# Kernel tuning notes

Hardware: AMD Instinct MI355X
Metric: run time of the kernel (lower is better)

The kernel has to match this reference:

```python
import jax, jax.numpy as jnp
import numpy as np
from jax import lax

STRIDE = 2
PAD = 1
KT = 3   # conv_transpose kernel
KP = 6   # fused pool window/stride (2*3)

def setup_inputs() -> dict:
    key = jax.random.key(0)
    kx, kw, kb = jax.random.split(key, 3)
    x = jax.random.normal(kx, (8, 32, 32, 32, 32), dtype=jnp.float32)
    W = jax.random.normal(kw, (32, 16, KT, KT, KT), dtype=jnp.float32) * 0.05
    b = jax.random.normal(kb, (16,), dtype=jnp.float32) * 0.05
    return {"x": x, "W": W, "b": b}

def _conv_transpose3d(x, W, b):
    # PyTorch conv_transpose3d: weight (C_in, C_out, k, k, k)
    # equivalent to conv with lhs dilation, flipped kernel, swapped I/O axes
    w2 = jnp.flip(W, axis=(2, 3, 4)).swapaxes(0, 1)  # (C_out, C_in, k, k, k)
    pad = KT - 1 - PAD
    y = lax.conv_general_dilated(
        x, w2,
        window_strides=(1, 1, 1),
        padding=[(pad, pad)] * 3,
        lhs_dilation=(STRIDE, STRIDE, STRIDE),
        dimension_numbers=("NCDHW", "OIDHW", "NCDHW"),
    )
    return y + b[None, :, None, None, None]

def reference(x, W, b):
    y = _conv_transpose3d(x, W, b)  # (N, C_out, 63, 63, 63)
    # fused maxpool(k=2,s=2) + maxpool(k=3,s=3) == maxpool(k=6,s=6)
    pooled = lax.reduce_window(
        y, -jnp.inf, lax.max,
        window_dimensions=(1, 1, KP, KP, KP),
        window_strides=(1, 1, KP, KP, KP),
        padding="VALID",
    )  # (N, C_out, 10, 10, 10)
    return jnp.sum(pooled, axis=1, keepdims=True)  # (N, 1, 10, 10, 10)
```

## Files before the change

kernel.cpp:

```cpp
#include <hip/hip_runtime.h>

typedef __bf16 bf16;
typedef __bf16 bf16x8 __attribute__((ext_vector_type(8)));
typedef float f32x4 __attribute__((ext_vector_type(4)));

#define CI_STRIDE 40
#define IW_STRIDE (CI_STRIDE)
#define IH_STRIDE (17 * CI_STRIDE)
#define ID_STRIDE (5 * 17 * CI_STRIDE)
#define XS_ELEMS (4 * ID_STRIDE)

__global__ void transpose_w_kernel(const float* __restrict__ W, bf16* __restrict__ Wt) {
  int o = blockIdx.x * 256 + threadIdx.x;
  if (o < 27 * 512) {
    int j = o & 7, co = (o >> 3) & 15, q = (o >> 7) & 3, tap = o >> 9;
    int ci = q * 8 + j;
    Wt[o] = (bf16)W[(ci * 16 + co) * 27 + tap];
  }
}

__global__ __launch_bounds__(128) void fused_mfma_kernel(
    const float* __restrict__ x, const bf16* __restrict__ Wt,
    const float* __restrict__ b, float* __restrict__ out) {
  __shared__ __align__(16) bf16 xs[XS_ELEMS];
  __shared__ float red[5][2][16];

  const int t = threadIdx.x;
  const int lane = t & 63;
  const int wv = t >> 6;
  const int co = lane & 15;
  const int quad = lane >> 4;

  const int blk = blockIdx.x;
  const int nodoh = blk >> 1;
  const int half = blk & 1;
  const int n = nodoh / 100;
  const int od = (nodoh / 10) % 10;
  const int oh = nodoh % 10;

  bf16x8 bfrag[27];
  {
    const bf16x8* wp = (const bf16x8*)Wt;
#pragma unroll
    for (int tap = 0; tap < 27; ++tap)
      bfrag[tap] = wp[(tap * 4 + quad) * 16 + co];
  }

  {
    const float* xn = x + (size_t)n * (32 * 32768) + (3 * od) * 1024 + (3 * oh) * 32 + 15 * half;
    for (int i = t; i < 512 * 16; i += 128) {
      int w = i & 15;
      int row = i >> 4;
      int ci = row >> 4, ld = (row >> 2) & 3, lh = row & 3;
      float v = xn[ci * 32768 + ld * 1024 + lh * 32 + w];
      xs[(size_t)ld * ID_STRIDE + lh * IH_STRIDE + w * IW_STRIDE + ci] = (bf16)v;
    }
  }
  __syncthreads();

  for (int i = 0; i < 5; ++i) {
    const int tau = wv + 2 * i;
    const int w5 = tau >> 1;
    const int tb = (tau & 1) * 16;

    int pos = tb + (lane & 15);
    if (pos > 26) pos = 26;
    const int md = pos / 9;
    const int rem = pos - md * 9;
    const int mh = rem / 3;
    const int mw = rem - mh * 3;
    const bf16* ap = xs + (size_t)md * ID_STRIDE + mh * IH_STRIDE +
                     (3 * w5 + mw) * IW_STRIDE + quad * 8;

    bf16x8 af[8];
#pragma unroll
    for (int dd = 0; dd < 2; ++dd)
#pragma unroll
      for (int dh = 0; dh < 2; ++dh)
#pragma unroll
        for (int dw = 0; dw < 2; ++dw)
          af[dd * 4 + dh * 2 + dw] =
              *(const bf16x8*)(ap + dd * ID_STRIDE + dh * IH_STRIDE + dw * IW_STRIDE);

    float tmax = -3.4e38f;
#pragma unroll
    for (int pd = 0; pd < 2; ++pd)
#pragma unroll
      for (int ph = 0; ph < 2; ++ph)
#pragma unroll
        for (int pw = 0; pw < 2; ++pw) {
          f32x4 acc = {0.f, 0.f, 0.f, 0.f};
#pragma unroll
          for (int td = 0; td <= pd; ++td)
#pragma unroll
            for (int th = 0; th <= ph; ++th)
#pragma unroll
              for (int tw = 0; tw <= pw; ++tw) {
                const int kd = pd ? (td ? 2 : 0) : 1;
                const int kh = ph ? (th ? 2 : 0) : 1;
                const int kw = pw ? (tw ? 2 : 0) : 1;
                const int tap = kd * 9 + kh * 3 + kw;
                const int ai = ((kd == 0) ? 4 : 0) + ((kh == 0) ? 2 : 0) + ((kw == 0) ? 1 : 0);
                acc = __builtin_amdgcn_mfma_f32_16x16x32_bf16(af[ai], bfrag[tap], acc, 0, 0, 0);
              }
#pragma unroll
          for (int r = 0; r < 4; ++r) {
            if (tb + quad * 4 + r < 27) tmax = fmaxf(tmax, acc[r]);
          }
        }

    tmax = fmaxf(tmax, __shfl_xor(tmax, 16, 64));
    tmax = fmaxf(tmax, __shfl_xor(tmax, 32, 64));
    if (quad == 0) red[w5][tau & 1][co] = tmax;
  }
  __syncthreads();

  if (t < 80) {
    const int w5 = t >> 4;
    const int c = t & 15;
    float v = fmaxf(red[w5][0][c], red[w5][1][c]) + b[c];
    v += __shfl_xor(v, 1, 64);
    v += __shfl_xor(v, 2, 64);
    v += __shfl_xor(v, 4, 64);
    v += __shfl_xor(v, 8, 64);
    if (c == 0) out[nodoh * 10 + half * 5 + w5] = v;
  }
}

extern "C" void kernel_launch(void* const* d_in, const int* in_sizes, int n_in,
                              void* d_out, int out_size, void* d_ws, size_t ws_size,
                              hipStream_t stream) {
  const float* x = (const float*)d_in[0];
  const float* W = (const float*)d_in[1];
  const float* b = (const float*)d_in[2];
  float* out = (float*)d_out;
  bf16* Wt = (bf16*)d_ws;

  transpose_w_kernel<<<dim3(54), dim3(256), 0, stream>>>(W, Wt);
  fused_mfma_kernel<<<dim3(1600), dim3(128), 0, stream>>>(x, Wt, b, out);
}
```

Before: 98.28 us.

## Merge half-width blocks into full-row 256-thread blocks with vectorized LDS staging

Each block now covers the full 32-wide input row (all 10 output columns) with 4 waves instead of two blocks covering halves with 2 waves. This removes the overlapping halo load between the two halves. Each wave keeps a fixed M-tile, so position decoding is hoisted out of the loop. The staging loop now gathers 8 channels per thread and writes one bf16x8 to LDS instead of scalar bf16 stores. The cost is half as many blocks (800) and twice the LDS per block, which may lower occupancy or parallelism.

```diff
diff --git a/kernel.cpp b/kernel.cpp
--- a/kernel.cpp
+++ b/kernel.cpp
@@ -4,26 +4,24 @@
 typedef __bf16 bf16x8 __attribute__((ext_vector_type(8)));
 typedef float f32x4 __attribute__((ext_vector_type(4)));
 
-#define CI_STRIDE 40
-#define IW_STRIDE (CI_STRIDE)
-#define IH_STRIDE (17 * CI_STRIDE)
-#define ID_STRIDE (5 * 17 * CI_STRIDE)
-#define XS_ELEMS (4 * ID_STRIDE)
+#define W_STRIDE 40
+#define H_STRIDE (33 * W_STRIDE)
+#define D_STRIDE (5 * H_STRIDE)
+#define XS_ELEMS (4 * D_STRIDE)
 
 __global__ void transpose_w_kernel(const float* __restrict__ W, bf16* __restrict__ Wt) {
   int o = blockIdx.x * 256 + threadIdx.x;
   if (o < 27 * 512) {
     int j = o & 7, co = (o >> 3) & 15, q = (o >> 7) & 3, tap = o >> 9;
-    int ci = q * 8 + j;
-    Wt[o] = (bf16)W[(ci * 16 + co) * 27 + tap];
+    Wt[o] = (bf16)W[((q * 8 + j) * 16 + co) * 27 + tap];
   }
 }
 
-__global__ __launch_bounds__(128) void fused_mfma_kernel(
+__global__ __launch_bounds__(256) void fused_mfma_kernel(
     const float* __restrict__ x, const bf16* __restrict__ Wt,
     const float* __restrict__ b, float* __restrict__ out) {
   __shared__ __align__(16) bf16 xs[XS_ELEMS];
-  __shared__ float red[5][2][16];
+  __shared__ float red[10][2][16];
 
   const int t = threadIdx.x;
   const int lane = t & 63;
@@ -32,11 +30,9 @@
   const int quad = lane >> 4;
 
   const int blk = blockIdx.x;
-  const int nodoh = blk >> 1;
-  const int half = blk & 1;
-  const int n = nodoh / 100;
-  const int od = (nodoh / 10) % 10;
-  const int oh = nodoh % 10;
+  const int n = blk / 100;
+  const int od = (blk / 10) % 10;
+  const int oh = blk % 10;
 
   bf16x8 bfrag[27];
   {
@@ -47,30 +43,35 @@
   }
 
   {
-    const float* xn = x + (size_t)n * (32 * 32768) + (3 * od) * 1024 + (3 * oh) * 32 + 15 * half;
-    for (int i = t; i < 512 * 16; i += 128) {
-      int w = i & 15;
-      int row = i >> 4;
-      int ci = row >> 4, ld = (row >> 2) & 3, lh = row & 3;
-      float v = xn[ci * 32768 + ld * 1024 + lh * 32 + w];
-      xs[(size_t)ld * ID_STRIDE + lh * IH_STRIDE + w * IW_STRIDE + ci] = (bf16)v;
+    const float* xn = x + (size_t)n * (32 * 32768) + (3 * od) * 1024 + (3 * oh) * 32;
+#pragma unroll 2
+    for (int it = 0; it < 8; ++it) {
+      const int flat = it * 256 + t;
+      const int w = flat & 31;
+      const int row = flat >> 5;
+      const int cig = row & 3;
+      const int lh = (row >> 2) & 3;
+      const int ld = row >> 4;
+      const float* g = xn + (size_t)(cig * 8) * 32768 + ld * 1024 + lh * 32 + w;
+      bf16x8 pk;
+#pragma unroll
+      for (int j = 0; j < 8; ++j) pk[j] = (bf16)g[(size_t)j * 32768];
+      *(bf16x8*)&xs[ld * D_STRIDE + lh * H_STRIDE + w * W_STRIDE + cig * 8] = pk;
     }
   }
   __syncthreads();
 
+  const int tile = wv >> 1;
+  const int tb = tile * 16;
+  int pos = tb + (lane & 15);
+  if (pos > 26) pos = 26;
+  const int md = pos / 9;
+  const int mh = (pos / 3) % 3;
+  const int mw = pos % 3;
+
   for (int i = 0; i < 5; ++i) {
-    const int tau = wv + 2 * i;
-    const int w5 = tau >> 1;
-    const int tb = (tau & 1) * 16;
-
-    int pos = tb + (lane & 15);
-    if (pos > 26) pos = 26;
-    const int md = pos / 9;
-    const int rem = pos - md * 9;
-    const int mh = rem / 3;
-    const int mw = rem - mh * 3;
-    const bf16* ap = xs + (size_t)md * ID_STRIDE + mh * IH_STRIDE +
-                     (3 * w5 + mw) * IW_STRIDE + quad * 8;
+    const int w10 = (wv & 1) * 5 + i;
+    const bf16* ap = xs + md * D_STRIDE + mh * H_STRIDE + (3 * w10 + mw) * W_STRIDE + quad * 8;
 
     bf16x8 af[8];
 #pragma unroll
@@ -80,7 +81,7 @@
 #pragma unroll
         for (int dw = 0; dw < 2; ++dw)
           af[dd * 4 + dh * 2 + dw] =
-              *(const bf16x8*)(ap + dd * ID_STRIDE + dh * IH_STRIDE + dw * IW_STRIDE);
+              *(const bf16x8*)(ap + dd * D_STRIDE + dh * H_STRIDE + dw * W_STRIDE);
 
     float tmax = -3.4e38f;
 #pragma unroll
@@ -99,31 +100,35 @@
                 const int kd = pd ? (td ? 2 : 0) : 1;
                 const int kh = ph ? (th ? 2 : 0) : 1;
                 const int kw = pw ? (tw ? 2 : 0) : 1;
-                const int tap = kd * 9 + kh * 3 + kw;
                 const int ai = ((kd == 0) ? 4 : 0) + ((kh == 0) ? 2 : 0) + ((kw == 0) ? 1 : 0);
-                acc = __builtin_amdgcn_mfma_f32_16x16x32_bf16(af[ai], bfrag[tap], acc, 0, 0, 0);
+                acc = __builtin_amdgcn_mfma_f32_16x16x32_bf16(
+                    af[ai], bfrag[kd * 9 + kh * 3 + kw], acc, 0, 0, 0);
               }
+          if (tile == 0) {
 #pragma unroll
-          for (int r = 0; r < 4; ++r) {
-            if (tb + quad * 4 + r < 27) tmax = fmaxf(tmax, acc[r]);
+            for (int r = 0; r < 4; ++r) tmax = fmaxf(tmax, acc[r]);
+          } else {
+#pragma unroll
+            for (int r = 0; r < 4; ++r)
+              if (16 + quad * 4 + r < 27) tmax = fmaxf(tmax, acc[r]);
           }
         }
 
     tmax = fmaxf(tmax, __shfl_xor(tmax, 16, 64));
     tmax = fmaxf(tmax, __shfl_xor(tmax, 32, 64));
-    if (quad == 0) red[w5][tau & 1][co] = tmax;
+    if (quad == 0) red[w10][tile][co] = tmax;
   }
   __syncthreads();
 
-  if (t < 80) {
-    const int w5 = t >> 4;
+  if (t < 160) {
+    const int w10 = t >> 4;
     const int c = t & 15;
-    float v = fmaxf(red[w5][0][c], red[w5][1][c]) + b[c];
+    float v = fmaxf(red[w10][0][c], red[w10][1][c]) + b[c];
     v += __shfl_xor(v, 1, 64);
     v += __shfl_xor(v, 2, 64);
     v += __shfl_xor(v, 4, 64);
     v += __shfl_xor(v, 8, 64);
-    if (c == 0) out[nodoh * 10 + half * 5 + w5] = v;
+    if (c == 0) out[blk * 10 + w10] = v;
   }
 }
 
@@ -137,5 +142,5 @@
   bf16* Wt = (bf16*)d_ws;
 
   transpose_w_kernel<<<dim3(54), dim3(256), 0, stream>>>(W, Wt);
-  fused_mfma_kernel<<<dim3(1600), dim3(128), 0, stream>>>(x, Wt, b, out);
+  fused_mfma_kernel<<<dim3(800), dim3(256), 0, stream>>>(x, Wt, b, out);
 }
```

Result: faster. 92.19 us (-6.2%).
